# Kernel tuning notes

Hardware: AMD Instinct MI355X
Metric: run time of the kernel (lower is better)

Reference implementation:

```python
import jax, jax.numpy as jnp
import numpy as np

B, LQ, LA, D, H = 8, 2048, 2048, 300, 150

def setup_inputs() -> dict:
    key = jax.random.key(0)
    ks = jax.random.split(key, 6)
    return {
        "Q": jax.random.normal(ks[0], (B, LQ, D), dtype=jnp.float32),
        "A": jax.random.normal(ks[1], (B, LA, D), dtype=jnp.float32),
        "Wi": jax.random.normal(ks[2], (D, H), dtype=jnp.float32) * (1.0 / np.sqrt(D)),
        "Wu": jax.random.normal(ks[3], (D, H), dtype=jnp.float32) * (1.0 / np.sqrt(D)),
        "Wg": jax.random.normal(ks[4], (H, H), dtype=jnp.float32) * (1.0 / np.sqrt(H)),
        "Wt": jax.random.normal(ks[5], (2 * H, H), dtype=jnp.float32) * (1.0 / np.sqrt(2 * H)),
        "bi": jnp.zeros((H,), dtype=jnp.float32),
        "bu": jnp.zeros((H,), dtype=jnp.float32),
        "bg": jnp.zeros((H,), dtype=jnp.float32),
        "bt": jnp.zeros((H,), dtype=jnp.float32),
    }

def reference(Q, A, Wi, Wu, Wg, Wt, bi, bu, bg, bt):
    # sigmoid/tanh gated projections (shared weights for Q and A)
    def gate(X):
        return jax.nn.sigmoid(X @ Wi + bi) * jnp.tanh(X @ Wu + bu)
    Qh = gate(Q)  # [B, LQ, H]
    Ah = gate(A)  # [B, LA, H]
    # attention scores G[b,q,a] = <(Qh Wg + bg)[b,q], Ah[b,a]>
    G = jnp.einsum('bqh,bah->bqa', Qh @ Wg + bg, Ah)
    G = jax.nn.softmax(G, axis=1)  # softmax over Q positions
    # H[b,a] = sum_q G[b,q,a] * Qh[b,q]
    Hm = jnp.einsum('bqa,bqh->bah', G, Qh)  # [B, LA, H]
    # 'nn' comparison: relu(concat([Ah, Hm]) @ Wt + bt)
    T = jax.nn.relu(jnp.concatenate([Ah, Hm], axis=-1) @ Wt + bt)
    return T
```

## Files before the change

kernel.cpp:

```cpp
#include <hip/hip_runtime.h>
#include <math.h>

#define BB 8
#define LQ 2048
#define DD 300
#define HHH 150
#define NROWS (BB * LQ)

#define KP 168
#define QTS 72
#define WCE 27136
#define SLAB_B 46080
#define SLAB_E 23040
#define QHT_OFF_E 11008

typedef __bf16 bf16x8 __attribute__((ext_vector_type(8)));
typedef __bf16 bf16x4 __attribute__((ext_vector_type(4)));
typedef float f32x16 __attribute__((ext_vector_type(16)));

__device__ __forceinline__ void gl_lds16(const void* g, void* l) {
    __builtin_amdgcn_global_load_lds(
        (const __attribute__((address_space(1))) void*)g,
        (__attribute__((address_space(3))) void*)l,
        16, 0, 0);
}
__device__ __forceinline__ void stage_flat(const void* g, void* l, int bytes,
                                           int w, int lane) {
    for (int ofs = w * 1024; ofs < bytes; ofs += 4096)
        gl_lds16((const char*)g + ofs + lane * 16, (char*)l + ofs);
}
__device__ __forceinline__ void stage_flat8(const void* g, void* l, int bytes,
                                            int w, int lane) {
    for (int ofs = w * 1024; ofs < bytes; ofs += 8192)
        gl_lds16((const char*)g + ofs + lane * 16, (char*)l + ofs);
}
__device__ __forceinline__ f32x16 z16() {
    f32x16 v;
#pragma unroll
    for (int i = 0; i < 16; i++) v[i] = 0.f;
    return v;
}
__device__ __forceinline__ bf16x8 cvt8(float4 u, float4 v) {
    return (bf16x8){(__bf16)u.x, (__bf16)u.y, (__bf16)u.z, (__bf16)u.w,
                    (__bf16)v.x, (__bf16)v.y, (__bf16)v.z, (__bf16)v.w};
}
__device__ __forceinline__ unsigned pk2(float lo, float hi) {
    unsigned d;
    asm("v_cvt_pk_bf16_f32 %0, %1, %2" : "=v"(d) : "v"(lo), "v"(hi));
    return d;
}
__device__ __forceinline__ void pl32(unsigned& a, unsigned& b) {
    asm("v_permlane32_swap_b32 %0, %1" : "+v"(a), "+v"(b));
}
__device__ __forceinline__ bf16x8 mk8(unsigned a, unsigned b, unsigned c, unsigned d) {
    union { unsigned u[4]; bf16x8 v; } x;
    x.u[0] = a; x.u[1] = b; x.u[2] = c; x.u[3] = d;
    return x.v;
}

__global__ __launch_bounds__(256) void convert_weights(
    const float* __restrict__ Wi, const float* __restrict__ Wu,
    const float* __restrict__ Wg, const float* __restrict__ Wt,
    __bf16* __restrict__ WiC, __bf16* __restrict__ WuC,
    __bf16* __restrict__ WgT, __bf16* __restrict__ Wt12)
{
    const int z = blockIdx.y;
    const int i = blockIdx.x * 256 + threadIdx.x;
    if (z < 2) {
        if (i >= 2 * WCE) return;
        int c = i / WCE, rem = i - c * WCE;
        float v = 0.f;
        if (rem < 160 * KP) {
            int h = rem / KP, kc = rem - h * KP;
            int d = c * 160 + kc;
            if (kc < 160 && d < DD && h < HHH) v = (z ? Wu : Wi)[(size_t)d * HHH + h];
        }
        (z ? WuC : WiC)[i] = (__bf16)v;
    } else if (z == 2) {
        if (i >= WCE) return;
        float v = 0.f;
        if (i < 160 * KP) {
            int h = i / KP, kc = i - h * KP;
            if (kc < HHH && h < HHH) v = Wg[(size_t)kc * HHH + h];
        }
        WgT[i] = (__bf16)v;
    } else {
        if (i >= 2 * 160 * KP) return;
        int c = i / (160 * KP), rem = i - c * (160 * KP);
        int h = rem / KP, kc = rem - h * KP;
        float v = (kc < HHH && h < HHH) ? Wt[(size_t)(c * HHH + kc) * HHH + h] : 0.f;
        Wt12[i] = (__bf16)v;
    }
}

__global__ __launch_bounds__(512, 2) void gatep(
    const float* __restrict__ Q, const float* __restrict__ A,
    const __bf16* __restrict__ WiC, const __bf16* __restrict__ WuC,
    const __bf16* __restrict__ WgT,
    const float* __restrict__ bi, const float* __restrict__ bu,
    const float* __restrict__ bg,
    __bf16* __restrict__ AhB, __bf16* __restrict__ Slab)
{
    __shared__ __align__(16) __bf16 WB[2][WCE];
    __shared__ __align__(16) __bf16 QhA[128 * KP];
    const int tid = threadIdx.x;
    const int w = tid >> 6, lane = tid & 63;
    const int m32 = lane & 31, half = lane >> 5;
    const int wm = w & 3, wn = w >> 2;
    const int tof = wn ? 3 : 0, tn = wn ? 2 : 3;
    const int z = blockIdx.y;
    const int r0 = blockIdx.x * 128;
    const float* X = z ? A : Q;

    stage_flat8(WiC, WB[0], 54272, w, lane);

    const float* xrow = X + (size_t)(r0 + wm * 32 + m32) * DD + half * 8;
    bf16x8 af0[10], af1[10];
#pragma unroll
    for (int ks = 0; ks < 10; ks++) {
        float4 u = *(const float4*)(xrow + ks * 16);
        float4 v = *(const float4*)(xrow + ks * 16 + 4);
        af0[ks] = cvt8(u, v);
    }

    f32x16 ai[3], au[3];
#pragma unroll
    for (int t = 0; t < 3; t++) { ai[t] = z16(); au[t] = z16(); }

    __syncthreads();
    stage_flat8(WuC, WB[1], 54272, w, lane);

#pragma unroll
    for (int ks = 0; ks < 8; ks++) {
        float4 u = *(const float4*)(xrow + 160 + ks * 16);
        float4 v = *(const float4*)(xrow + 160 + ks * 16 + 4);
        af1[ks] = cvt8(u, v);
    }
    {
        float4 u = *(const float4*)(xrow + 288);
        float4 v = (half == 0) ? *(const float4*)(xrow + 292) : (float4){0.f, 0.f, 0.f, 0.f};
        af1[8] = cvt8(u, v);
        af1[9] = (bf16x8){(__bf16)0.f, (__bf16)0.f, (__bf16)0.f, (__bf16)0.f,
                          (__bf16)0.f, (__bf16)0.f, (__bf16)0.f, (__bf16)0.f};
    }

    for (int ks = 0; ks < 10; ks++)
#pragma unroll
        for (int ti = 0; ti < 3; ti++)
            if (ti < tn)
                ai[ti] = __builtin_amdgcn_mfma_f32_32x32x16_bf16(
                    af0[ks], *(const bf16x8*)(WB[0] + ((tof + ti) * 32 + m32) * KP + ks * 16 + half * 8),
                    ai[ti], 0, 0, 0);
    __syncthreads();
    stage_flat8(WiC + WCE, WB[0], 54272, w, lane);
    for (int ks = 0; ks < 10; ks++)
#pragma unroll
        for (int ti = 0; ti < 3; ti++)
            if (ti < tn)
                au[ti] = __builtin_amdgcn_mfma_f32_32x32x16_bf16(
                    af0[ks], *(const bf16x8*)(WB[1] + ((tof + ti) * 32 + m32) * KP + ks * 16 + half * 8),
                    au[ti], 0, 0, 0);
    __syncthreads();
    stage_flat8(WuC + WCE, WB[1], 54272, w, lane);
    for (int ks = 0; ks < 10; ks++)
#pragma unroll
        for (int ti = 0; ti < 3; ti++)
            if (ti < tn)
                ai[ti] = __builtin_amdgcn_mfma_f32_32x32x16_bf16(
                    af1[ks], *(const bf16x8*)(WB[0] + ((tof + ti) * 32 + m32) * KP + ks * 16 + half * 8),
                    ai[ti], 0, 0, 0);
    __syncthreads();
    if (z == 0) stage_flat8(WgT, WB[0], 54272, w, lane);
    for (int ks = 0; ks < 10; ks++)
#pragma unroll
        for (int ti = 0; ti < 3; ti++)
            if (ti < tn)
                au[ti] = __builtin_amdgcn_mfma_f32_32x32x16_bf16(
                    af1[ks], *(const bf16x8*)(WB[1] + ((tof + ti) * 32 + m32) * KP + ks * 16 + half * 8),
                    au[ti], 0, 0, 0);

#pragma unroll
    for (int ti = 0; ti < 3; ti++) {
        if (ti >= tn) continue;
        int h = (tof + ti) * 32 + m32;
        int hc = h < HHH ? h : 0;
        float bih = bi[hc], buh = bu[hc];
#pragma unroll
        for (int r = 0; r < 16; r++) {
            float v = 0.f;
            if (h < HHH) {
                float xi = ai[ti][r] + bih, xu = au[ti][r] + buh;
                float s = 1.f / (1.f + __expf(-xi));
                float tt = 1.f - 2.f / (1.f + __expf(2.f * xu));
                v = s * tt;
            }
            ai[ti][r] = v;
        }
    }

    if (z) {
#pragma unroll
        for (int ti = 0; ti < 3; ti++) {
            if (ti >= tn) continue;
            int h = (tof + ti) * 32 + m32;
#pragma unroll
            for (int r = 0; r < 16; r++) {
                int rowp = (r & 3) + 8 * (r >> 2) + 4 * half;
                AhB[(size_t)(r0 + wm * 32 + rowp) * KP + h] = (__bf16)ai[ti][r];
            }
        }
        return;
    }

#pragma unroll
    for (int ti = 0; ti < 3; ti++) {
        if (ti >= tn) continue;
        int h = (tof + ti) * 32 + m32;
#pragma unroll
        for (int r = 0; r < 16; r++) {
            int rowp = (r & 3) + 8 * (r >> 2) + 4 * half;
            QhA[(wm * 32 + rowp) * KP + h] = (__bf16)ai[ti][r];
        }
    }
    __syncthreads();

    bf16x8 afq[10];
#pragma unroll
    for (int ks = 0; ks < 10; ks++)
        afq[ks] = *(const bf16x8*)(QhA + (wm * 32 + m32) * KP + ks * 16 + half * 8);

    f32x16 qg[3];
#pragma unroll
    for (int t = 0; t < 3; t++) qg[t] = z16();
    for (int ks = 0; ks < 10; ks++)
#pragma unroll
        for (int ti = 0; ti < 3; ti++)
            if (ti < tn)
                qg[ti] = __builtin_amdgcn_mfma_f32_32x32x16_bf16(
                    afq[ks], *(const bf16x8*)(WB[0] + ((tof + ti) * 32 + m32) * KP + ks * 16 + half * 8),
                    qg[ti], 0, 0, 0);

    const int b = r0 >> 11, qt0 = (r0 & 2047) >> 6;
#pragma unroll
    for (int ti = 0; ti < 3; ti++) {
        if (ti >= tn) continue;
        int h = (tof + ti) * 32 + m32;
        int hc = h < HHH ? h : 0;
        float bgh = bg[hc];
#pragma unroll
        for (int r = 0; r < 16; r++) {
            int rowp = (r & 3) + 8 * (r >> 2) + 4 * half;
            int q = (r0 & 2047) + wm * 32 + rowp;
            float v = (h < HHH) ? (qg[ti][r] + bgh) : 0.f;
            Slab[(size_t)(b * 32 + (q >> 6)) * SLAB_E + (q & 63) * KP + h] = (__bf16)v;
        }
    }

    {
        const int jl = tid & 63, tile = (tid >> 6) & 1, hgrp = tid >> 7;
        for (int hseg = hgrp; hseg < 20; hseg += 4) {
            bf16x8 vv = *(const bf16x8*)(QhA + (tile * 64 + jl) * KP + hseg * 8);
            __bf16* dst = Slab + (size_t)(b * 32 + qt0 + tile) * SLAB_E + QHT_OFF_E + jl;
#pragma unroll
            for (int e = 0; e < 8; e++)
                dst[(hseg * 8 + e) * QTS] = vv[e];
        }
    }
}

__global__ __launch_bounds__(512, 2) void attn_mfma(
    const __bf16* __restrict__ Slab, const __bf16* __restrict__ AhB,
    __bf16* __restrict__ O, float* __restrict__ L)
{
    __shared__ __align__(16) __bf16 Buf[3][SLAB_E];
    const int tid = threadIdx.x;
    const int w = tid >> 6, lane = tid & 63;
    const int m32 = lane & 31, half = lane >> 5;
    const int grp = blockIdx.x;
    const int b = grp >> 2, qp = grp & 3;
    const int a0 = blockIdx.y * 256;

    const char* slabBase = (const char*)Slab + (size_t)(b * 32 + qp * 8) * SLAB_B;
    stage_flat8(slabBase, Buf[0], SLAB_B, w, lane);
    __builtin_amdgcn_sched_barrier(0);

    const __bf16* arow = AhB + (size_t)(b * LQ + a0 + w * 32 + m32) * KP + half * 8;
    bf16x8 af[10];
#pragma unroll
    for (int ks = 0; ks < 10; ks++)
        af[ks] = *(const bf16x8*)(arow + ks * 16);
    __builtin_amdgcn_sched_barrier(0);

    stage_flat8(slabBase + SLAB_B, Buf[1], SLAB_B, w, lane);
    __builtin_amdgcn_sched_barrier(0);
    asm volatile("s_waitcnt vmcnt(15)" ::: "memory");
    __builtin_amdgcn_sched_barrier(0);
    __builtin_amdgcn_s_barrier();
    __builtin_amdgcn_sched_barrier(0);

    float lsum = 0.f;
    f32x16 acc[5];
#pragma unroll
    for (int t = 0; t < 5; t++) acc[t] = z16();

    for (int qt = 0; qt < 8; qt++) {
        if (qt < 6)
            stage_flat8(slabBase + (size_t)(qt + 2) * SLAB_B, Buf[(qt + 2) % 3],
                        SLAB_B, w, lane);
        const __bf16* Bq = Buf[qt % 3];
        const __bf16* Bv = Bq + QHT_OFF_E;

        f32x16 s0 = z16(), s1 = z16();
        __builtin_amdgcn_s_setprio(1);
        for (int ks = 0; ks < 10; ks++) {
            bf16x8 b0 = *(const bf16x8*)(Bq + m32 * KP + ks * 16 + half * 8);
            bf16x8 b1 = *(const bf16x8*)(Bq + (32 + m32) * KP + ks * 16 + half * 8);
            s0 = __builtin_amdgcn_mfma_f32_32x32x16_bf16(b0, af[ks], s0, 0, 0, 0);
            s1 = __builtin_amdgcn_mfma_f32_32x32x16_bf16(b1, af[ks], s1, 0, 0, 0);
        }
        __builtin_amdgcn_s_setprio(0);

#pragma unroll
        for (int r = 0; r < 16; r++) { s0[r] = __expf(s0[r]); lsum += s0[r]; }
#pragma unroll
        for (int r = 0; r < 16; r++) { s1[r] = __expf(s1[r]); lsum += s1[r]; }

        bf16x8 pf[4];
        {
            unsigned w01 = pk2(s0[0], s0[1]),   w45 = pk2(s0[4], s0[5]);
            unsigned w23 = pk2(s0[2], s0[3]),   w67 = pk2(s0[6], s0[7]);
            pl32(w01, w45); pl32(w23, w67);
            pf[0] = mk8(w01, w23, w45, w67);
            unsigned x01 = pk2(s0[8], s0[9]),   x45 = pk2(s0[12], s0[13]);
            unsigned x23 = pk2(s0[10], s0[11]), x67 = pk2(s0[14], s0[15]);
            pl32(x01, x45); pl32(x23, x67);
            pf[1] = mk8(x01, x23, x45, x67);
        }
        {
            unsigned w01 = pk2(s1[0], s1[1]),   w45 = pk2(s1[4], s1[5]);
            unsigned w23 = pk2(s1[2], s1[3]),   w67 = pk2(s1[6], s1[7]);
            pl32(w01, w45); pl32(w23, w67);
            pf[2] = mk8(w01, w23, w45, w67);
            unsigned x01 = pk2(s1[8], s1[9]),   x45 = pk2(s1[12], s1[13]);
            unsigned x23 = pk2(s1[10], s1[11]), x67 = pk2(s1[14], s1[15]);
            pl32(x01, x45); pl32(x23, x67);
            pf[3] = mk8(x01, x23, x45, x67);
        }

        __builtin_amdgcn_s_setprio(1);
#pragma unroll
        for (int kk = 0; kk < 4; kk++)
#pragma unroll
            for (int t = 0; t < 5; t++)
                acc[t] = __builtin_amdgcn_mfma_f32_32x32x16_bf16(
                    *(const bf16x8*)(Bv + (t * 32 + m32) * QTS + kk * 16 + half * 8),
                    pf[kk], acc[t], 0, 0, 0);
        __builtin_amdgcn_s_setprio(0);

        if (qt < 7) {
            __builtin_amdgcn_sched_barrier(0);
            if (qt < 6) asm volatile("s_waitcnt vmcnt(5)" ::: "memory");
            else        asm volatile("s_waitcnt vmcnt(0)" ::: "memory");
            __builtin_amdgcn_sched_barrier(0);
            __builtin_amdgcn_s_barrier();
            __builtin_amdgcn_sched_barrier(0);
        }
    }

    float lt = lsum + __shfl_xor(lsum, 32, 64);

    __bf16* Ob = O + ((size_t)qp * NROWS + b * LQ + a0 + w * 32) * 160;
#pragma unroll
    for (int t = 0; t < 5; t++)
#pragma unroll
        for (int rq = 0; rq < 4; rq++) {
            bf16x4 hv = {(__bf16)acc[t][rq * 4 + 0], (__bf16)acc[t][rq * 4 + 1],
                         (__bf16)acc[t][rq * 4 + 2], (__bf16)acc[t][rq * 4 + 3]};
            *(bf16x4*)(Ob + (size_t)m32 * 160 + t * 32 + rq * 8 + half * 4) = hv;
        }
    if (half == 0)
        L[(size_t)qp * NROWS + b * LQ + a0 + w * 32 + m32] = lt;
}

__global__ __launch_bounds__(256, 1) void final_mfma(
    const __bf16* __restrict__ AhB, const __bf16* __restrict__ O,
    const float* __restrict__ L, const __bf16* __restrict__ Wt12,
    const float* __restrict__ bt, float* __restrict__ Out)
{
    __shared__ __align__(16) __bf16 AS[64 * KP];
    __shared__ __align__(16) __bf16 HS[64 * KP];
    __shared__ __align__(16) __bf16 WtS[2 * 160 * KP];
    const int tid = threadIdx.x;
    const int w = tid >> 6, lane = tid & 63;
    const int m32 = lane & 31, half = lane >> 5;
    const int r0 = blockIdx.x * 64;

    stage_flat(AhB + (size_t)r0 * KP, AS, 21504, w, lane);
    stage_flat(Wt12, WtS, 107520, w, lane);

    {
        int rhat = tid >> 2, qq = tid & 3;
        int grow = r0 + rhat;
        float inv = 1.f / (L[grow] + L[NROWS + grow] + L[2 * NROWS + grow] + L[3 * NROWS + grow]);
#pragma unroll
        for (int k = 0; k < 5; k++) {
            float sum[8];
#pragma unroll
            for (int j = 0; j < 8; j++) sum[j] = 0.f;
#pragma unroll
            for (int p = 0; p < 4; p++) {
                bf16x8 x = *(const bf16x8*)(O + ((size_t)p * NROWS + grow) * 160 + qq * 40 + k * 8);
#pragma unroll
                for (int j = 0; j < 8; j++) sum[j] += (float)x[j];
            }
            bf16x8 hv;
#pragma unroll
            for (int j = 0; j < 8; j++) hv[j] = (__bf16)(sum[j] * inv);
            *(bf16x8*)(HS + rhat * KP + qq * 40 + k * 8) = hv;
        }
    }
    __syncthreads();

    const int m = w & 1, th = w >> 1;
    const int tbase = th ? 3 : 0, tn = th ? 2 : 3;
    f32x16 acc[3];
#pragma unroll
    for (int i = 0; i < 3; i++) acc[i] = z16();

    for (int ch = 0; ch < 2; ch++) {
        const __bf16* src = ch ? HS : AS;
        for (int ks = 0; ks < 10; ks++) {
            bf16x8 af = *(const bf16x8*)(src + (m * 32 + m32) * KP + ks * 16 + half * 8);
#pragma unroll
            for (int ti = 0; ti < 3; ti++) {
                if (ti < tn) {
                    int t = tbase + ti;
                    acc[ti] = __builtin_amdgcn_mfma_f32_32x32x16_bf16(
                        af, *(const bf16x8*)(WtS + (ch * 160 + t * 32 + m32) * KP + ks * 16 + half * 8),
                        acc[ti], 0, 0, 0);
                }
            }
        }
    }

#pragma unroll
    for (int ti = 0; ti < 3; ti++) {
        if (ti < tn) {
            int t = tbase + ti;
            int h = t * 32 + m32;
            if (h < HHH) {
                float bth = bt[h];
#pragma unroll
                for (int r = 0; r < 16; r++) {
                    int rowp = (r & 3) + 8 * (r >> 2) + 4 * half;
                    float v = acc[ti][r] + bth;
                    Out[(size_t)(r0 + m * 32 + rowp) * HHH + h] = v > 0.f ? v : 0.f;
                }
            }
        }
    }
}

extern "C" void kernel_launch(void* const* d_in, const int* in_sizes, int n_in,
                              void* d_out, int out_size, void* d_ws, size_t ws_size,
                              hipStream_t stream)
{
    const float* Q  = (const float*)d_in[0];
    const float* A  = (const float*)d_in[1];
    const float* Wi = (const float*)d_in[2];
    const float* Wu = (const float*)d_in[3];
    const float* Wg = (const float*)d_in[4];
    const float* Wt = (const float*)d_in[5];
    const float* bi = (const float*)d_in[6];
    const float* bu = (const float*)d_in[7];
    const float* bg = (const float*)d_in[8];
    const float* bt = (const float*)d_in[9];
    float* out = (float*)d_out;

    char* ws = (char*)d_ws;
    __bf16* Slab = (__bf16*)(ws);
    __bf16* AhB  = (__bf16*)(ws + 11796480);
    __bf16* Op   = (__bf16*)(ws + 17301504);
    float*  Lp   = (float*) (ws + 38273024);
    __bf16* WiC  = (__bf16*)(ws + 38535168);
    __bf16* WuC  = (__bf16*)(ws + 38643712);
    __bf16* WgT  = (__bf16*)(ws + 38752256);
    __bf16* Wt12 = (__bf16*)(ws + 38806528);

    convert_weights<<<dim3(212, 4), 256, 0, stream>>>(Wi, Wu, Wg, Wt,
                                                      WiC, WuC, WgT, Wt12);
    gatep<<<dim3(NROWS / 128, 2), 512, 0, stream>>>(Q, A, WiC, WuC, WgT,
                                                    bi, bu, bg, AhB, Slab);
    attn_mfma<<<dim3(32, 8), 512, 0, stream>>>(Slab, AhB, Op, Lp);
    final_mfma<<<NROWS / 64, 256, 0, stream>>>(AhB, Op, Lp, Wt12, bt, out);
}
```

Measured before the change: 160.1 us.

## Shrink gatep row tile and K-chunks to raise occupancy

Restructures the gate projection kernel so each block handles 64 rows instead of 128 and streams weights in four 80-wide K chunks instead of two 160-wide ones. The smaller LDS footprint and fewer accumulators per wave let launch bounds request 4 blocks per CU, and the grid doubles. The Wg projection is also split into two chunks with double buffering. The cost is more barriers and staging rounds, redundant weight loads per row processed, and a reworked weight packing layout.

Measured after the change: 209.5 us. +30.8%, slower.

```diff
diff --git a/kernel.cpp b/kernel.cpp
--- a/kernel.cpp
+++ b/kernel.cpp
@@ -9,7 +9,9 @@
 
 #define KP 168
 #define QTS 72
-#define WCE 27136
+#define KQ 88
+#define WCQ 14336
+#define STG_B 28160
 #define SLAB_B 46080
 #define SLAB_E 23040
 #define QHT_OFF_E 11008
@@ -67,21 +69,23 @@
     const int z = blockIdx.y;
     const int i = blockIdx.x * 256 + threadIdx.x;
     if (z < 2) {
-        if (i >= 2 * WCE) return;
-        int c = i / WCE, rem = i - c * WCE;
+        if (i >= 4 * WCQ) return;
+        int c = i / WCQ, rem = i - c * WCQ;
         float v = 0.f;
-        if (rem < 160 * KP) {
-            int h = rem / KP, kc = rem - h * KP;
-            int d = c * 160 + kc;
-            if (kc < 160 && d < DD && h < HHH) v = (z ? Wu : Wi)[(size_t)d * HHH + h];
+        if (rem < 160 * KQ) {
+            int h = rem / KQ, kc = rem - h * KQ;
+            int d = c * 80 + kc;
+            if (kc < 80 && d < DD && h < HHH) v = (z ? Wu : Wi)[(size_t)d * HHH + h];
         }
         (z ? WuC : WiC)[i] = (__bf16)v;
     } else if (z == 2) {
-        if (i >= WCE) return;
+        if (i >= 2 * WCQ) return;
+        int c = i / WCQ, rem = i - c * WCQ;
         float v = 0.f;
-        if (i < 160 * KP) {
-            int h = i / KP, kc = i - h * KP;
-            if (kc < HHH && h < HHH) v = Wg[(size_t)kc * HHH + h];
+        if (rem < 160 * KQ) {
+            int h = rem / KQ, kc = rem - h * KQ;
+            int k = c * 80 + kc;
+            if (kc < 80 && k < HHH && h < HHH) v = Wg[(size_t)k * HHH + h];
         }
         WgT[i] = (__bf16)v;
     } else {
@@ -93,7 +97,19 @@
     }
 }
 
-__global__ __launch_bounds__(512, 2) void gatep(
+#define GPH(ACC, C, BUF)                                                      \
+    for (int ks = 0; ks < 5; ks++) {                                          \
+        _Pragma("unroll")                                                     \
+        for (int ti = 0; ti < 2; ti++)                                        \
+            if (ti < tn)                                                      \
+                ACC[ti] = __builtin_amdgcn_mfma_f32_32x32x16_bf16(            \
+                    af[C][ks],                                                \
+                    *(const bf16x8*)(WB[BUF] + ((tof + ti) * 32 + m32) * KQ + \
+                                     ks * 16 + half * 8),                     \
+                    ACC[ti], 0, 0, 0);                                        \
+    }
+
+__global__ __launch_bounds__(512, 4) void gatep(
     const float* __restrict__ Q, const float* __restrict__ A,
     const __bf16* __restrict__ WiC, const __bf16* __restrict__ WuC,
     const __bf16* __restrict__ WgT,
@@ -101,86 +117,71 @@
     const float* __restrict__ bg,
     __bf16* __restrict__ AhB, __bf16* __restrict__ Slab)
 {
-    __shared__ __align__(16) __bf16 WB[2][WCE];
-    __shared__ __align__(16) __bf16 QhA[128 * KP];
+    __shared__ __align__(16) __bf16 WB[2][WCQ];
+    __shared__ __align__(16) __bf16 QhA[64 * KP];
     const int tid = threadIdx.x;
     const int w = tid >> 6, lane = tid & 63;
     const int m32 = lane & 31, half = lane >> 5;
-    const int wm = w & 3, wn = w >> 2;
-    const int tof = wn ? 3 : 0, tn = wn ? 2 : 3;
+    const int wm = w & 1, wn = w >> 1;
+    const int tof = (wn == 0) ? 0 : wn + 1;
+    const int tn = (wn == 0) ? 2 : 1;
     const int z = blockIdx.y;
-    const int r0 = blockIdx.x * 128;
+    const int r0 = blockIdx.x * 64;
     const float* X = z ? A : Q;
 
-    stage_flat8(WiC, WB[0], 54272, w, lane);
-
-    const float* xrow = X + (size_t)(r0 + wm * 32 + m32) * DD + half * 8;
-    bf16x8 af0[10], af1[10];
-#pragma unroll
-    for (int ks = 0; ks < 10; ks++) {
-        float4 u = *(const float4*)(xrow + ks * 16);
-        float4 v = *(const float4*)(xrow + ks * 16 + 4);
-        af0[ks] = cvt8(u, v);
-    }
-
-    f32x16 ai[3], au[3];
-#pragma unroll
-    for (int t = 0; t < 3; t++) { ai[t] = z16(); au[t] = z16(); }
-
-    __syncthreads();
-    stage_flat8(WuC, WB[1], 54272, w, lane);
-
-#pragma unroll
-    for (int ks = 0; ks < 8; ks++) {
-        float4 u = *(const float4*)(xrow + 160 + ks * 16);
-        float4 v = *(const float4*)(xrow + 160 + ks * 16 + 4);
-        af1[ks] = cvt8(u, v);
-    }
-    {
-        float4 u = *(const float4*)(xrow + 288);
-        float4 v = (half == 0) ? *(const float4*)(xrow + 292) : (float4){0.f, 0.f, 0.f, 0.f};
-        af1[8] = cvt8(u, v);
-        af1[9] = (bf16x8){(__bf16)0.f, (__bf16)0.f, (__bf16)0.f, (__bf16)0.f,
-                          (__bf16)0.f, (__bf16)0.f, (__bf16)0.f, (__bf16)0.f};
-    }
-
-    for (int ks = 0; ks < 10; ks++)
-#pragma unroll
-        for (int ti = 0; ti < 3; ti++)
-            if (ti < tn)
-                ai[ti] = __builtin_amdgcn_mfma_f32_32x32x16_bf16(
-                    af0[ks], *(const bf16x8*)(WB[0] + ((tof + ti) * 32 + m32) * KP + ks * 16 + half * 8),
-                    ai[ti], 0, 0, 0);
-    __syncthreads();
-    stage_flat8(WiC + WCE, WB[0], 54272, w, lane);
-    for (int ks = 0; ks < 10; ks++)
-#pragma unroll
-        for (int ti = 0; ti < 3; ti++)
-            if (ti < tn)
-                au[ti] = __builtin_amdgcn_mfma_f32_32x32x16_bf16(
-                    af0[ks], *(const bf16x8*)(WB[1] + ((tof + ti) * 32 + m32) * KP + ks * 16 + half * 8),
-                    au[ti], 0, 0, 0);
-    __syncthreads();
-    stage_flat8(WuC + WCE, WB[1], 54272, w, lane);
-    for (int ks = 0; ks < 10; ks++)
-#pragma unroll
-        for (int ti = 0; ti < 3; ti++)
-            if (ti < tn)
-                ai[ti] = __builtin_amdgcn_mfma_f32_32x32x16_bf16(
-                    af1[ks], *(const bf16x8*)(WB[0] + ((tof + ti) * 32 + m32) * KP + ks * 16 + half * 8),
-                    ai[ti], 0, 0, 0);
-    __syncthreads();
-    if (z == 0) stage_flat8(WgT, WB[0], 54272, w, lane);
-    for (int ks = 0; ks < 10; ks++)
-#pragma unroll
-        for (int ti = 0; ti < 3; ti++)
-            if (ti < tn)
-                au[ti] = __builtin_amdgcn_mfma_f32_32x32x16_bf16(
-                    af1[ks], *(const bf16x8*)(WB[1] + ((tof + ti) * 32 + m32) * KP + ks * 16 + half * 8),
-                    au[ti], 0, 0, 0);
-
-#pragma unroll
-    for (int ti = 0; ti < 3; ti++) {
+    stage_flat8(WiC, WB[0], STG_B, w, lane);
+
+    const float* xrow = X + (size_t)(r0 + wm * 32 + m32) * DD;
+    bf16x8 af[4][5];
+    const float4 zf = {0.f, 0.f, 0.f, 0.f};
+#pragma unroll
+    for (int c = 0; c < 4; c++)
+#pragma unroll
+        for (int ks = 0; ks < 5; ks++) {
+            const int colb = c * 80 + ks * 16;
+            const int col = colb + half * 8;
+            float4 u = zf, v = zf;
+            if (colb + 15 < DD) {
+                u = *(const float4*)(xrow + col);
+                v = *(const float4*)(xrow + col + 4);
+            } else if (colb < DD) {
+                if (col + 4 <= DD) u = *(const float4*)(xrow + col);
+                if (col + 8 <= DD) v = *(const float4*)(xrow + col + 4);
+            }
+            af[c][ks] = cvt8(u, v);
+        }
+
+    f32x16 ai[2], au[2];
+#pragma unroll
+    for (int t = 0; t < 2; t++) { ai[t] = z16(); au[t] = z16(); }
+
+    __syncthreads();
+    stage_flat8(WuC, WB[1], STG_B, w, lane);
+    GPH(ai, 0, 0);
+    __syncthreads();
+    stage_flat8(WiC + WCQ, WB[0], STG_B, w, lane);
+    GPH(au, 0, 1);
+    __syncthreads();
+    stage_flat8(WuC + WCQ, WB[1], STG_B, w, lane);
+    GPH(ai, 1, 0);
+    __syncthreads();
+    stage_flat8(WiC + 2 * WCQ, WB[0], STG_B, w, lane);
+    GPH(au, 1, 1);
+    __syncthreads();
+    stage_flat8(WuC + 2 * WCQ, WB[1], STG_B, w, lane);
+    GPH(ai, 2, 0);
+    __syncthreads();
+    stage_flat8(WiC + 3 * WCQ, WB[0], STG_B, w, lane);
+    GPH(au, 2, 1);
+    __syncthreads();
+    stage_flat8(WuC + 3 * WCQ, WB[1], STG_B, w, lane);
+    GPH(ai, 3, 0);
+    __syncthreads();
+    if (z == 0) stage_flat8(WgT, WB[0], STG_B, w, lane);
+    GPH(au, 3, 1);
+
+#pragma unroll
+    for (int ti = 0; ti < 2; ti++) {
         if (ti >= tn) continue;
         int h = (tof + ti) * 32 + m32;
         int hc = h < HHH ? h : 0;
@@ -200,7 +201,7 @@
 
     if (z) {
 #pragma unroll
-        for (int ti = 0; ti < 3; ti++) {
+        for (int ti = 0; ti < 2; ti++) {
             if (ti >= tn) continue;
             int h = (tof + ti) * 32 + m32;
 #pragma unroll
@@ -213,7 +214,7 @@
     }
 
 #pragma unroll
-    for (int ti = 0; ti < 3; ti++) {
+    for (int ti = 0; ti < 2; ti++) {
         if (ti >= tn) continue;
         int h = (tof + ti) * 32 + m32;
 #pragma unroll
@@ -224,25 +225,40 @@
     }
     __syncthreads();
 
-    bf16x8 afq[10];
-#pragma unroll
-    for (int ks = 0; ks < 10; ks++)
-        afq[ks] = *(const bf16x8*)(QhA + (wm * 32 + m32) * KP + ks * 16 + half * 8);
-
-    f32x16 qg[3];
-#pragma unroll
-    for (int t = 0; t < 3; t++) qg[t] = z16();
-    for (int ks = 0; ks < 10; ks++)
-#pragma unroll
-        for (int ti = 0; ti < 3; ti++)
+    stage_flat8(WgT + WCQ, WB[1], STG_B, w, lane);
+
+    bf16x8 afq[2][5];
+#pragma unroll
+    for (int s = 0; s < 2; s++)
+#pragma unroll
+        for (int ks = 0; ks < 5; ks++)
+            afq[s][ks] = *(const bf16x8*)(QhA + (wm * 32 + m32) * KP +
+                                          s * 80 + ks * 16 + half * 8);
+
+    f32x16 qg[2];
+#pragma unroll
+    for (int t = 0; t < 2; t++) qg[t] = z16();
+    for (int ks = 0; ks < 5; ks++)
+#pragma unroll
+        for (int ti = 0; ti < 2; ti++)
             if (ti < tn)
                 qg[ti] = __builtin_amdgcn_mfma_f32_32x32x16_bf16(
-                    afq[ks], *(const bf16x8*)(WB[0] + ((tof + ti) * 32 + m32) * KP + ks * 16 + half * 8),
+                    afq[0][ks],
+                    *(const bf16x8*)(WB[0] + ((tof + ti) * 32 + m32) * KQ + ks * 16 + half * 8),
                     qg[ti], 0, 0, 0);
+    __syncthreads();
+    for (int ks = 0; ks < 5; ks++)
+#pragma unroll
+        for (int ti = 0; ti < 2; ti++)
+            if (ti < tn)
+                qg[ti] = __builtin_amdgcn_mfma_f32_32x32x16_bf16(
+                    afq[1][ks],
+                    *(const bf16x8*)(WB[1] + ((tof + ti) * 32 + m32) * KQ + ks * 16 + half * 8),
+                    qg[ti], 0, 0, 0);
 
     const int b = r0 >> 11, qt0 = (r0 & 2047) >> 6;
 #pragma unroll
-    for (int ti = 0; ti < 3; ti++) {
+    for (int ti = 0; ti < 2; ti++) {
         if (ti >= tn) continue;
         int h = (tof + ti) * 32 + m32;
         int hc = h < HHH ? h : 0;
@@ -250,17 +266,17 @@
 #pragma unroll
         for (int r = 0; r < 16; r++) {
             int rowp = (r & 3) + 8 * (r >> 2) + 4 * half;
-            int q = (r0 & 2047) + wm * 32 + rowp;
+            int ql = wm * 32 + rowp;
             float v = (h < HHH) ? (qg[ti][r] + bgh) : 0.f;
-            Slab[(size_t)(b * 32 + (q >> 6)) * SLAB_E + (q & 63) * KP + h] = (__bf16)v;
+            Slab[(size_t)(b * 32 + qt0) * SLAB_E + ql * KP + h] = (__bf16)v;
         }
     }
 
     {
-        const int jl = tid & 63, tile = (tid >> 6) & 1, hgrp = tid >> 7;
-        for (int hseg = hgrp; hseg < 20; hseg += 4) {
-            bf16x8 vv = *(const bf16x8*)(QhA + (tile * 64 + jl) * KP + hseg * 8);
-            __bf16* dst = Slab + (size_t)(b * 32 + qt0 + tile) * SLAB_E + QHT_OFF_E + jl;
+        const int jl = tid & 63, hgrp = tid >> 6;
+        __bf16* dst = Slab + (size_t)(b * 32 + qt0) * SLAB_E + QHT_OFF_E + jl;
+        for (int hseg = hgrp; hseg < 20; hseg += 8) {
+            bf16x8 vv = *(const bf16x8*)(QhA + jl * KP + hseg * 8);
 #pragma unroll
             for (int e = 0; e < 8; e++)
                 dst[(hseg * 8 + e) * QTS] = vv[e];
@@ -483,14 +499,14 @@
     __bf16* Op   = (__bf16*)(ws + 17301504);
     float*  Lp   = (float*) (ws + 38273024);
     __bf16* WiC  = (__bf16*)(ws + 38535168);
-    __bf16* WuC  = (__bf16*)(ws + 38643712);
-    __bf16* WgT  = (__bf16*)(ws + 38752256);
-    __bf16* Wt12 = (__bf16*)(ws + 38806528);
-
-    convert_weights<<<dim3(212, 4), 256, 0, stream>>>(Wi, Wu, Wg, Wt,
+    __bf16* WuC  = (__bf16*)(ws + 38649856);
+    __bf16* WgT  = (__bf16*)(ws + 38764544);
+    __bf16* Wt12 = (__bf16*)(ws + 38821888);
+
+    convert_weights<<<dim3(224, 4), 256, 0, stream>>>(Wi, Wu, Wg, Wt,
                                                       WiC, WuC, WgT, Wt12);
-    gatep<<<dim3(NROWS / 128, 2), 512, 0, stream>>>(Q, A, WiC, WuC, WgT,
-                                                    bi, bu, bg, AhB, Slab);
+    gatep<<<dim3(NROWS / 64, 2), 512, 0, stream>>>(Q, A, WiC, WuC, WgT,
+                                                   bi, bu, bg, AhB, Slab);
     attn_mfma<<<dim3(32, 8), 512, 0, stream>>>(Slab, AhB, Op, Lp);
     final_mfma<<<NROWS / 64, 256, 0, stream>>>(AhB, Op, Lp, Wt12, bt, out);
 }
```
